# Optimization experiments

Hardware: AMD Instinct MI355X
Metric: run time of the kernel (lower is better)

The kernel has to match this reference:

```python
import jax, jax.numpy as jnp
import numpy as np


def gcn(adj_bin, x, W, b):
    # torch_geometric GCNConv with add_self_loops=True, no edge_weight (binary adj)
    N = adj_bin.shape[-1]
    A = adj_bin + jnp.eye(N, dtype=adj_bin.dtype)
    d = A.sum(-1)
    dis = jnp.where(d > 0, jax.lax.rsqrt(jnp.maximum(d, 1e-12)), 0.0)
    norm = dis[..., :, None] * A * dis[..., None, :]
    return jnp.einsum('bij,bjh->bih', norm, x @ W) + b


def normalize_batch_adj(adj):
    # CoarsenBlock.normalize_batch_adj on weighted dense adjacency
    N = adj.shape[-1]
    A = adj + jnp.eye(N, dtype=adj.dtype)
    dis = jnp.clip(A.sum(-1), 1.0, None) ** -0.5
    newA = dis[..., :, None] * A * dis[..., None, :]
    return (adj.sum(-1) > 0).astype(adj.dtype)[..., None] * newA


def cut_and_mask(alpha, num_sent, k):
    # get_topk_range_for_sentences: walk alpha in descending order until k
    # indices that are sentence nodes (index < num_sent) have been seen.
    N = alpha.shape[0]
    order = jnp.argsort(-alpha)  # descending
    csum = jnp.cumsum((order < num_sent).astype(jnp.int32))
    pos = jnp.argmax(csum >= k)  # first position where k sentences seen
    cut = alpha[order[pos]]
    sorted_mask = (jnp.arange(N) <= pos).astype(alpha.dtype)
    index_mask = jnp.zeros_like(alpha).at[order].set(sorted_mask)
    return cut, index_mask


def setup_inputs() -> dict:
    key = jax.random.key(0)
    ks = jax.random.split(key, 8)
    B, N, F, H = 16, 1024, 768, 128
    x = jax.random.normal(ks[0], (B, N, F), jnp.float32)
    w = jax.random.uniform(ks[1], (B, N, N), jnp.float32)
    m = jax.random.uniform(ks[2], (B, N, N)) < 0.03  # ~30 avg degree
    adj = jnp.where(m, w, 0.0)
    num_sentences = jax.random.randint(ks[3], (B,), 4, N + 1).astype(jnp.int32)
    W1 = jax.random.normal(ks[4], (F, H), jnp.float32) / np.float32(np.sqrt(F))
    b1 = jnp.zeros((H,), jnp.float32)
    Watt = jax.random.normal(ks[5], (H, 1), jnp.float32) / np.float32(np.sqrt(H))
    batt = jnp.zeros((1,), jnp.float32)
    W2 = jax.random.normal(ks[6], (H, F), jnp.float32) / np.float32(np.sqrt(H))
    b2 = jnp.zeros((F,), jnp.float32)
    return dict(x=x, adj=adj, num_sentences=num_sentences, W1=W1, b1=b1,
                Watt=Watt, batt=batt, W2=W2, b2=b2, num_output_sentences=3)


def reference(x, adj, num_sentences, W1, b1, Watt, batt, W2, b2, num_output_sentences):
    adj_bin = (adj > 0).astype(x.dtype)
    # embed_block1 + relu
    x1 = jax.nn.relu(gcn(adj_bin, x, W1, b1))  # [B,N,H]
    # attention: sigmoid(gcn_att(x1)^2)
    alpha = jax.nn.sigmoid(gcn(adj_bin, x1, Watt, batt) ** 2)[..., 0]  # [B,N]
    norm_adj = normalize_batch_adj(adj)  # [B,N,N]
    cut, index_mask = jax.vmap(cut_and_mask, in_axes=(0, 0, None))(
        alpha, num_sentences, num_output_sentences)
    cut_alpha = jax.nn.relu(alpha + 1e-7 - cut[:, None])  # [B,N]
    S = norm_adj * cut_alpha[:, None, :]
    # F.normalize(S, p=1, dim=-1)
    S = S / jnp.clip(jnp.abs(S).sum(-1, keepdims=True), 1e-12, None)
    # coarsening matmuls
    coarse_x = jnp.einsum('bij,bif->bjf', S, x1)        # S^T x1
    StA = jnp.einsum('bji,bjk->bik', S, adj)            # S^T A
    coarse_adj = jnp.einsum('bik,bkl->bil', StA, S)     # S^T A S
    coarse_adj = jnp.floor(coarse_adj * 1e4) / 1e4      # floor quantization, 4 digits
    # embed_block2 + tanh on the coarse graph (binary coarse adjacency)
    coarse_bin = (coarse_adj != 0).astype(x.dtype)
    x2 = jnp.tanh(gcn(coarse_bin, coarse_x, W2, b2))    # [B,N,F]
    xs0 = coarse_x.mean(-1)
    xs1 = x2.mean(-1)
    return (x2, coarse_x, coarse_adj, S, index_mask, xs0, xs1)
```

## Files before the change

### kernel.cpp

```cpp
#include <hip/hip_runtime.h>

#define B_ 16
#define N_ 1024
#define F_ 768
#define H_ 128

typedef float f32x4 __attribute__((ext_vector_type(4)));
typedef short s16x8 __attribute__((ext_vector_type(8)));
typedef unsigned short u16;
typedef u16 u16x8 __attribute__((ext_vector_type(8)));
typedef u16 u16x4 __attribute__((ext_vector_type(4)));
typedef unsigned long long u64;

__device__ __forceinline__ u16 f2b(float f) {
  unsigned u = __float_as_uint(f);
  unsigned r = (u + 0x7FFFu + ((u >> 16) & 1u)) >> 16;
  return (u16)r;
}
__device__ __forceinline__ float b2f(u16 u) {
  return __uint_as_float(((unsigned)u) << 16);
}

__device__ __forceinline__ void gload16(const u16* g, u16* l) {
  __builtin_amdgcn_global_load_lds(
      (const __attribute__((address_space(1))) unsigned int*)g,
      (__attribute__((address_space(3))) unsigned int*)l, 16, 0, 0);
}

__device__ __forceinline__ float ftanh(float z) {
  z = fminf(fmaxf(z, -10.0f), 10.0f);
  float e = __expf(2.0f * z);
  return (e - 1.0f) / (e + 1.0f);
}

__device__ __forceinline__ float blockReduceSum256(float v) {
  __shared__ float red[4];
  #pragma unroll
  for (int o = 32; o > 0; o >>= 1) v += __shfl_down(v, o, 64);
  if ((threadIdx.x & 63) == 0) red[threadIdx.x >> 6] = v;
  __syncthreads();
  float r = red[0] + red[1] + red[2] + red[3];
  __syncthreads();
  return r;
}

__global__ __launch_bounds__(256) void k_prep(
    const float* __restrict__ X, u16* __restrict__ Yh, u16* __restrict__ Ym,
    u16* __restrict__ Yl, long n4,
    const float* __restrict__ W1, u16* __restrict__ W1h,
    u16* __restrict__ W1m, u16* __restrict__ W1l,
    const float* __restrict__ adj, float* __restrict__ dis_bin,
    float* __restrict__ dr, float* __restrict__ dc, u64* __restrict__ bm,
    u16* __restrict__ adj_bf, int* __restrict__ rowcnt,
    float* __restrict__ xs0, float* __restrict__ xs1) {
  __shared__ float tile[32][33];
  int tid = threadIdx.x;
  if (blockIdx.x < 2048) {
    long i = (long)blockIdx.x * 256 + tid;
    long stride = 2048L * 256;
    for (; i < n4; i += stride) {
      f32x4 v = *(const f32x4*)(X + i * 4);
      u16x4 oh, om, ol;
      #pragma unroll
      for (int e = 0; e < 4; ++e) {
        float f = v[e];
        u16 h = f2b(f); float r1 = f - b2f(h);
        u16 m = f2b(r1); float r2 = r1 - b2f(m);
        u16 l = f2b(r2);
        oh[e] = h; om[e] = m; ol[e] = l;
      }
      *(u16x4*)(Yh + i * 4) = oh;
      *(u16x4*)(Ym + i * 4) = om;
      *(u16x4*)(Yl + i * 4) = ol;
    }
  } else if (blockIdx.x < 2144) {
    int bid = blockIdx.x - 2048;
    int bx = bid & 3, by = bid >> 2;
    int tx = tid & 31, ty = tid >> 5;
    int r0 = by * 32, c0 = bx * 32;
    #pragma unroll
    for (int i = 0; i < 4; ++i)
      tile[ty + i * 8][tx] = W1[(long)(r0 + ty + i * 8) * H_ + (c0 + tx)];
    __syncthreads();
    #pragma unroll
    for (int i = 0; i < 4; ++i) {
      float v = tile[tx][ty + i * 8];
      long o = (long)(c0 + ty + i * 8) * F_ + (r0 + tx);
      u16 h = f2b(v); float r1 = v - b2f(h);
      u16 m = f2b(r1); float r2 = r1 - b2f(m);
      u16 l = f2b(r2);
      W1h[o] = h; W1m[o] = m; W1l[o] = l;
    }
  } else {
    long row = blockIdx.x - 2144;
    const float* a = adj + row * N_;
    u16* ab = adj_bf + row * N_;
    float cnt = 0.f, sw = 0.f;
    #pragma unroll
    for (int it = 0; it < 4; ++it) {
      int j = tid + it * 256;
      float v = a[j];
      ab[j] = f2b(v);
      bool nz = (v != 0.0f);
      u64 ball = __ballot(nz);
      if ((tid & 63) == 0) bm[row * 16 + it * 4 + (tid >> 6)] = ball;
      if (nz) { cnt += 1.0f; sw += v; }
    }
    __shared__ float r1[4], r2[4];
    #pragma unroll
    for (int o = 32; o > 0; o >>= 1) { cnt += __shfl_down(cnt, o, 64); sw += __shfl_down(sw, o, 64); }
    if ((tid & 63) == 0) { r1[tid >> 6] = cnt; r2[tid >> 6] = sw; }
    __syncthreads();
    if (tid == 0) {
      float c = r1[0] + r1[1] + r1[2] + r1[3];
      float s = r2[0] + r2[1] + r2[2] + r2[3];
      dis_bin[row] = rsqrtf(c + 1.0f);
      float d = rsqrtf(s + 1.0f);
      dc[row] = d;
      dr[row] = (s > 0.0f) ? d : 0.0f;
      rowcnt[row] = 0;
      xs0[row] = 0.0f;
      xs1[row] = 0.0f;
    }
  }
}

template<int NPLANES, int MODE>
__global__ __launch_bounds__(256) void mgemmW(
    const u16* __restrict__ A0, const u16* __restrict__ A1, const u16* __restrict__ A2,
    const u16* __restrict__ B0, const u16* __restrict__ B1, const u16* __restrict__ B2,
    float* __restrict__ C, int N, int K, long sA, long sB, long sC,
    u16* __restrict__ Cbf, float* __restrict__ xsum) {
  int bz = blockIdx.z;
  int m0 = blockIdx.y * 128, n0 = blockIdx.x * 64;
  __shared__ __align__(16) u16 As[NPLANES][128 * 32];
  __shared__ __align__(16) u16 Bs[NPLANES][64 * 32];
  int tid = threadIdx.x;
  int lane = tid & 63, wave = tid >> 6;
  int wr = wave >> 1, wc = wave & 1;
  int kg = lane >> 4, r16 = lane & 15;
  const u16* Aps[3] = {A0, A1, A2};
  const u16* Bps[3] = {B0, B1, B2};
  const u16* ga[NPLANES];
  const u16* gb[NPLANES];
  #pragma unroll
  for (int p2 = 0; p2 < NPLANES; ++p2) {
    ga[p2] = Aps[p2] + (long)bz * sA + (long)(m0 + (tid >> 2)) * K + (tid & 3) * 8;
    gb[p2] = Bps[p2] + (long)bz * sB + (long)(n0 + (tid >> 2)) * K + (tid & 3) * 8;
  }
  f32x4 acc[4][2] = {};

  for (int k0 = 0; k0 < K; k0 += 32) {
    #pragma unroll
    for (int p2 = 0; p2 < NPLANES; ++p2) {
      gload16(ga[p2] + k0, &As[p2][tid * 8]);
      gload16(ga[p2] + (long)64 * K + k0, &As[p2][2048 + tid * 8]);
      gload16(gb[p2] + k0, &Bs[p2][tid * 8]);
    }
    __syncthreads();
    s16x8 af[NPLANES][4], bf[NPLANES][2];
    #pragma unroll
    for (int p2 = 0; p2 < NPLANES; ++p2) {
      #pragma unroll
      for (int m = 0; m < 4; ++m)
        af[p2][m] = *(const s16x8*)(&As[p2][(wr * 64 + m * 16 + r16) * 32 + kg * 8]);
      #pragma unroll
      for (int n = 0; n < 2; ++n)
        bf[p2][n] = *(const s16x8*)(&Bs[p2][(wc * 32 + n * 16 + r16) * 32 + kg * 8]);
    }
    #pragma unroll
    for (int m = 0; m < 4; ++m)
      #pragma unroll
      for (int n = 0; n < 2; ++n) {
        acc[m][n] = __builtin_amdgcn_mfma_f32_16x16x32_bf16(af[0][m], bf[0][n], acc[m][n], 0, 0, 0);
        if constexpr (NPLANES == 3) {
          acc[m][n] = __builtin_amdgcn_mfma_f32_16x16x32_bf16(af[0][m], bf[1][n], acc[m][n], 0, 0, 0);
          acc[m][n] = __builtin_amdgcn_mfma_f32_16x16x32_bf16(af[1][m], bf[0][n], acc[m][n], 0, 0, 0);
          acc[m][n] = __builtin_amdgcn_mfma_f32_16x16x32_bf16(af[1][m], bf[1][n], acc[m][n], 0, 0, 0);
          acc[m][n] = __builtin_amdgcn_mfma_f32_16x16x32_bf16(af[0][m], bf[2][n], acc[m][n], 0, 0, 0);
          acc[m][n] = __builtin_amdgcn_mfma_f32_16x16x32_bf16(af[2][m], bf[0][n], acc[m][n], 0, 0, 0);
        }
      }
    __syncthreads();
  }

  #pragma unroll
  for (int m = 0; m < 4; ++m)
    #pragma unroll
    for (int r = 0; r < 4; ++r) {
      int row = m0 + wr * 64 + m * 16 + kg * 4 + r;
      float part = 0.f;
      #pragma unroll
      for (int n = 0; n < 2; ++n) {
        int col = n0 + wc * 32 + n * 16 + r16;
        long cidx = (long)bz * sC + (long)row * N + col;
        float v = acc[m][n][r];
        C[cidx] = v;
        if constexpr (MODE == 1) { Cbf[cidx] = f2b(v); part += v; }
      }
      if constexpr (MODE == 1) {
        #pragma unroll
        for (int o2 = 1; o2 < 16; o2 <<= 1) part += __shfl_xor(part, o2, 64);
        if (r16 == 0) atomicAdd(&xsum[(long)bz * N_ + row], part * (1.0f / H_));
      }
    }
}

__global__ __launch_bounds__(256) void k_G5G6(
    const u16* __restrict__ St, const u16* __restrict__ x1T,
    float* __restrict__ out_cx, u16* __restrict__ cx_bf,
    float* __restrict__ xs0,
    const u16* __restrict__ adjBF, u16* __restrict__ M1t) {
  __shared__ __align__(16) u16 smem[128 * 64];
  const long NN = (long)N_ * N_;
  const long NH = (long)N_ * H_;
  int tid = threadIdx.x;
  int lane = tid & 63, wave = tid >> 6;
  int wr = wave >> 1, wc = wave & 1;
  int kg = lane >> 4, r16 = lane & 15;

  if ((int)blockIdx.x < 256) {
    int id = blockIdx.x;
    int bxg = id & 1, byg = (id >> 1) & 7, bz = id >> 4;
    int m0 = byg * 128, n0 = bxg * 64;
    u16* As = smem;
    u16* Bs = smem + 128 * 32;
    const u16* ga = St + (long)bz * NN + (long)(m0 + (tid >> 2)) * N_ + (tid & 3) * 8;
    const u16* gb = x1T + (long)bz * NH + (long)(n0 + (tid >> 2)) * N_ + (tid & 3) * 8;
    f32x4 acc[4][2] = {};
    for (int k0 = 0; k0 < N_; k0 += 32) {
      gload16(ga + k0, &As[tid * 8]);
      gload16(ga + (long)64 * N_ + k0, &As[2048 + tid * 8]);
      gload16(gb + k0, &Bs[tid * 8]);
      __syncthreads();
      s16x8 af[4], bf[2];
      #pragma unroll
      for (int m = 0; m < 4; ++m)
        af[m] = *(const s16x8*)(&As[(wr * 64 + m * 16 + r16) * 32 + kg * 8]);
      #pragma unroll
      for (int n = 0; n < 2; ++n)
        bf[n] = *(const s16x8*)(&Bs[(wc * 32 + n * 16 + r16) * 32 + kg * 8]);
      #pragma unroll
      for (int m = 0; m < 4; ++m)
        #pragma unroll
        for (int n = 0; n < 2; ++n)
          acc[m][n] = __builtin_amdgcn_mfma_f32_16x16x32_bf16(af[m], bf[n], acc[m][n], 0, 0, 0);
      __syncthreads();
    }
    #pragma unroll
    for (int m = 0; m < 4; ++m)
      #pragma unroll
      for (int r = 0; r < 4; ++r) {
        int row = m0 + wr * 64 + m * 16 + kg * 4 + r;
        float part = 0.f;
        #pragma unroll
        for (int n = 0; n < 2; ++n) {
          int col = n0 + wc * 32 + n * 16 + r16;
          long cidx = (long)bz * NH + (long)row * H_ + col;
          float v = acc[m][n][r];
          out_cx[cidx] = v;
          cx_bf[cidx] = f2b(v);
          part += v;
        }
        #pragma unroll
        for (int o2 = 1; o2 < 16; o2 <<= 1) part += __shfl_xor(part, o2, 64);
        if (r16 == 0) atomicAdd(&xs0[(long)bz * N_ + row], part * (1.0f / H_));
      }
  } else {
    int lin = (int)blockIdx.x - 256;
    int swz = (lin & 7) * 128 + (lin >> 3);
    int bx = swz & 7, by = (swz >> 3) & 7, bz = swz >> 6;
    int m0 = by * 128, n0 = bx * 128;
    u16* As = smem;
    u16* Bs = smem + 128 * 32;
    const u16* ga = St + (long)bz * NN + (long)(m0 + (tid >> 2)) * N_ + (tid & 3) * 8;
    const u16* gb = adjBF + (long)bz * NN + (long)(n0 + (tid >> 2)) * N_ + (tid & 3) * 8;
    f32x4 acc[4][4] = {};
    for (int k0 = 0; k0 < N_; k0 += 32) {
      gload16(ga + k0, &As[tid * 8]);
      gload16(ga + (long)64 * N_ + k0, &As[2048 + tid * 8]);
      gload16(gb + k0, &Bs[tid * 8]);
      gload16(gb + (long)64 * N_ + k0, &Bs[2048 + tid * 8]);
      __syncthreads();
      s16x8 af[4], bfr[4];
      #pragma unroll
      for (int m = 0; m < 4; ++m)
        af[m] = *(const s16x8*)(&As[(wr * 64 + m * 16 + r16) * 32 + kg * 8]);
      #pragma unroll
      for (int n = 0; n < 4; ++n)
        bfr[n] = *(const s16x8*)(&Bs[(wc * 64 + n * 16 + r16) * 32 + kg * 8]);
      #pragma unroll
      for (int m = 0; m < 4; ++m)
        #pragma unroll
        for (int n = 0; n < 4; ++n)
          acc[m][n] = __builtin_amdgcn_mfma_f32_16x16x32_bf16(af[m], bfr[n], acc[m][n], 0, 0, 0);
      __syncthreads();
    }
    #pragma unroll
    for (int m = 0; m < 4; ++m)
      #pragma unroll
      for (int r = 0; r < 4; ++r) {
        int row = m0 + wr * 64 + m * 16 + kg * 4 + r;
        #pragma unroll
        for (int n = 0; n < 4; ++n) {
          int col = n0 + wc * 64 + n * 16 + r16;
          M1t[(long)bz * NN + (long)row * N_ + col] = f2b(acc[m][n][r]);
        }
      }
  }
}

__global__ __launch_bounds__(256) void k_spmm_relu(
    const u64* __restrict__ bm, const float* __restrict__ P1,
    const float* __restrict__ dis_bin, const float* __restrict__ b1,
    const float* __restrict__ Watt, float* __restrict__ x1,
    float* __restrict__ t) {
  long row = blockIdx.x;
  int b = (int)(row >> 10), i = (int)(row & 1023);
  const float* Pb = P1 + (long)b * (long)N_ * H_;
  const float* db = dis_bin + (long)b * N_;
  __shared__ int idxs[N_];
  __shared__ int wtot[4];
  __shared__ float accs[H_];
  int tid = threadIdx.x;
  int wid = tid >> 6, lane = tid & 63;
  int base = tid * 4;
  u64 word = bm[row * 16 + (tid >> 4)];
  int sh = base & 63;
  int f0 = (int)((word >> sh) & 1), f1 = (int)((word >> (sh + 1)) & 1);
  int f2 = (int)((word >> (sh + 2)) & 1), f3 = (int)((word >> (sh + 3)) & 1);
  int c0 = f0 + f1 + f2 + f3;
  int inc = c0;
  #pragma unroll
  for (int o = 1; o < 64; o <<= 1) {
    int v = __shfl_up(inc, o, 64);
    if (lane >= o) inc += v;
  }
  if (lane == 63) wtot[wid] = inc;
  __syncthreads();
  int wbase = 0;
  #pragma unroll
  for (int w = 0; w < 4; ++w) wbase += (w < wid) ? wtot[w] : 0;
  int pos = wbase + inc - c0;
  int n = wtot[0] + wtot[1] + wtot[2] + wtot[3];
  if (f0) idxs[pos++] = base;
  if (f1) idxs[pos++] = base + 1;
  if (f2) idxs[pos++] = base + 2;
  if (f3) idxs[pos++] = base + 3;
  __syncthreads();
  int c = tid & 127, team = tid >> 7;
  float acc = 0.f;
  for (int u = team; u < n; u += 2) {
    int j = idxs[u];
    acc += db[j] * Pb[(long)j * H_ + c];
  }
  if (team == 1) accs[c] = acc;
  __syncthreads();
  float v = 0.f;
  if (team == 0) {
    float di = db[i];
    float tot = acc + accs[c] + di * Pb[(long)i * H_ + c];
    v = fmaxf(di * tot + b1[c], 0.0f);
    x1[row * H_ + c] = v;
  }
  __syncthreads();
  float prod = (team == 0) ? v * Watt[c] : 0.f;
  float s = blockReduceSum256(prod);
  if (tid == 0) t[row] = s;
}

__global__ __launch_bounds__(256) void k_alpha(
    const u64* __restrict__ bm, const float* __restrict__ dis_bin,
    const float* __restrict__ t, const float* __restrict__ batt,
    float* __restrict__ alpha) {
  long row = blockIdx.x;
  int b = (int)(row >> 10), i = (int)(row & 1023);
  const float* db = dis_bin + (long)b * N_;
  const float* tb = t + (long)b * N_;
  int tid = threadIdx.x;
  float s = 0.f;
  #pragma unroll
  for (int it = 0; it < 4; ++it) {
    int j = tid + it * 256;
    u64 word = bm[row * 16 + (j >> 6)];
    if ((word >> (j & 63)) & 1) s += db[j] * tb[j];
  }
  s = blockReduceSum256(s);
  if (tid == 0) {
    float di = db[i];
    float pre = di * (s + di * tb[i]) + batt[0];
    float z = pre * pre;
    alpha[row] = 1.0f / (1.0f + expf(-z));
  }
}

__global__ __launch_bounds__(1024) void k_cutmask2(
    const float* __restrict__ alpha, const int* __restrict__ num_sent,
    const int* __restrict__ nout, float* __restrict__ index_mask,
    float* __restrict__ ca) {
  int b = blockIdx.x, tid = threadIdx.x;
  __shared__ u64 keys[N_];
  __shared__ u64 red[N_];
  int ns = num_sent[b];
  float av = alpha[(long)b * N_ + tid];
  unsigned bits = __float_as_uint(av);
  u64 keyFull = ((u64)bits << 32) | (u64)(0xFFFFFFFFu - (unsigned)tid);
  keys[tid] = (tid < ns) ? keyFull : 0ULL;
  __syncthreads();
  int k = nout[0];
  u64 cutkey = 0;
  for (int r = 0; r < k; ++r) {
    red[tid] = keys[tid];
    __syncthreads();
    for (int off = 512; off > 0; off >>= 1) {
      if (tid < off) { u64 o = red[tid + off]; if (o > red[tid]) red[tid] = o; }
      __syncthreads();
    }
    u64 mx = red[0];
    __syncthreads();
    if (r == k - 1) cutkey = mx;
    else if (keys[tid] == mx) keys[tid] = 0ULL;
    __syncthreads();
  }
  float cutalpha = __uint_as_float((unsigned)(cutkey >> 32));
  index_mask[(long)b * N_ + tid] = (keyFull >= cutkey) ? 1.0f : 0.0f;
  ca[(long)b * N_ + tid] = fmaxf(av + 1e-7f - cutalpha, 0.0f);
}

__global__ __launch_bounds__(256) void k_build_S(
    const u16* __restrict__ abf, const float* __restrict__ dr,
    const float* __restrict__ dc, const float* __restrict__ ca,
    float* __restrict__ S) {
  long row = blockIdx.x;
  int b = (int)(row >> 10), i = (int)(row & 1023);
  const u16* a = abf + row * N_;
  const float* dcb = dc + (long)b * N_;
  const float* cab = ca + (long)b * N_;
  float dri = dr[row];
  int tid = threadIdx.x;
  u16x4 av4 = *(const u16x4*)(a + tid * 4);
  f32x4 dc4 = *(const f32x4*)(dcb + tid * 4);
  f32x4 ca4 = *(const f32x4*)(cab + tid * 4);
  float ls = 0.f;
  f32x4 pv;
  #pragma unroll
  for (int e = 0; e < 4; ++e) {
    int j = tid * 4 + e;
    float avv = b2f(av4[e]) + ((j == i) ? 1.0f : 0.0f);
    float v = dri * avv * dc4[e] * ca4[e];
    pv[e] = v;
    ls += v;
  }
  float sum = blockReduceSum256(ls);
  float denom = fmaxf(sum, 1e-12f);
  f32x4 out;
  #pragma unroll
  for (int e = 0; e < 4; ++e) out[e] = pv[e] / denom;
  *(f32x4*)(&S[row * N_ + tid * 4]) = out;
}

__device__ __forceinline__ void convT_body(
    const float* __restrict__ Xb, u16* __restrict__ Yb, int R, int C,
    int r0, int c0, float tile[32][33]) {
  int tx = threadIdx.x & 31, ty = threadIdx.x >> 5;
  #pragma unroll
  for (int i = 0; i < 4; ++i)
    tile[ty + i * 8][tx] = Xb[(long)(r0 + ty + i * 8) * C + (c0 + tx)];
  __syncthreads();
  #pragma unroll
  for (int i = 0; i < 4; ++i)
    Yb[(long)(c0 + ty + i * 8) * R + (r0 + tx)] = f2b(tile[tx][ty + i * 8]);
}

__global__ __launch_bounds__(256) void k_convTall(
    const float* __restrict__ S, u16* __restrict__ St,
    const float* __restrict__ x1, u16* __restrict__ x1T,
    const float* __restrict__ W2, u16* __restrict__ W2T) {
  __shared__ float tile[32][33];
  long NN = (long)N_ * N_;
  long NH = (long)N_ * H_;
  int id = blockIdx.x;
  if (id < 16384) {
    int bx = id & 31, by = (id >> 5) & 31, bz = id >> 10;
    convT_body(S + (long)bz * NN, St + (long)bz * NN, N_, N_, by * 32, bx * 32, tile);
  } else if (id < 18432) {
    int id2 = id - 16384;
    int bx = id2 & 3, by = (id2 >> 2) & 31, bz = id2 >> 7;
    convT_body(x1 + (long)bz * NH, x1T + (long)bz * NH, N_, H_, by * 32, bx * 32, tile);
  } else {
    int id3 = id - 18432;
    int bx = id3 % 24, by = id3 / 24;
    convT_body(W2, W2T, H_, F_, by * 32, bx * 32, tile);
  }
}

template<int MODE>
__global__ __launch_bounds__(256) void mgemm(
    const u16* __restrict__ A, const u16* __restrict__ Bt, void* __restrict__ Cv,
    int M, int N, int K, long sA, long sB, long sC, long ldb,
    const int* __restrict__ cnt, const float* __restrict__ bias,
    int* __restrict__ rowcnt, u16* __restrict__ cbin,
    float* __restrict__ xsum) {
  int gx = gridDim.x, gy = gridDim.y;
  int lin = (blockIdx.z * gy + blockIdx.y) * gx + blockIdx.x;
  int total = gx * gy * gridDim.z;
  int chunk = total >> 3;
  int swz = (lin & 7) * chunk + (lin >> 3);
  int bx = swz % gx; int t2 = swz / gx; int by = t2 % gy; int bz = t2 / gy;

  int m0 = by * 128, n0 = bx * 128;
  const u16* Ab = A + (long)bz * sA + (long)m0 * K;
  const u16* Bb = Bt + (long)bz * sB + (long)n0 * ldb;
  __shared__ __align__(16) u16 As[128 * 32];
  __shared__ __align__(16) u16 Bs[128 * 32];
  int tid = threadIdx.x;
  int lane = tid & 63, wave = tid >> 6;
  int wr = wave >> 1, wc = wave & 1;
  int kg = lane >> 4, r16 = lane & 15;
  const u16* ga = Ab + (long)(tid >> 2) * K + (tid & 3) * 8;
  const u16* gb = Bb + (long)(tid >> 2) * ldb + (tid & 3) * 8;
  f32x4 acc[4][4] = {};

  for (int k0 = 0; k0 < K; k0 += 32) {
    gload16(ga + k0, &As[tid * 8]);
    gload16(ga + (long)64 * K + k0, &As[2048 + tid * 8]);
    gload16(gb + k0, &Bs[tid * 8]);
    gload16(gb + (long)64 * ldb + k0, &Bs[2048 + tid * 8]);
    __syncthreads();
    s16x8 af[4], bfr[4];
    #pragma unroll
    for (int m = 0; m < 4; ++m)
      af[m] = *(const s16x8*)(&As[(wr * 64 + m * 16 + r16) * 32 + kg * 8]);
    #pragma unroll
    for (int n = 0; n < 4; ++n)
      bfr[n] = *(const s16x8*)(&Bs[(wc * 64 + n * 16 + r16) * 32 + kg * 8]);
    #pragma unroll
    for (int m = 0; m < 4; ++m)
      #pragma unroll
      for (int n = 0; n < 4; ++n)
        acc[m][n] = __builtin_amdgcn_mfma_f32_16x16x32_bf16(af[m], bfr[n], acc[m][n], 0, 0, 0);
    __syncthreads();
  }

  if constexpr (MODE == 2) {
    int* cntl = (int*)As;
    if (tid < 128) cntl[tid] = 0;
    __syncthreads();
    #pragma unroll
    for (int m = 0; m < 4; ++m) {
      #pragma unroll
      for (int r = 0; r < 4; ++r) {
        int lrow = wr * 64 + m * 16 + kg * 4 + r;
        int row = m0 + lrow;
        int nz = 0;
        #pragma unroll
        for (int n = 0; n < 4; ++n) {
          int col = n0 + wc * 64 + n * 16 + r16;
          float q = floorf(acc[m][n][r] * 10000.0f) / 10000.0f;
          long cidx = (long)bz * sC + (long)row * N + col;
          ((float*)Cv)[cidx] = q;
          bool qnz = (q != 0.0f);
          u16 bv;
          if (row == col) bv = qnz ? (u16)0x4000 : (u16)0x3F80;
          else            bv = qnz ? (u16)0x3F80 : (u16)0;
          cbin[cidx] = bv;
          nz += qnz ? 1 : 0;
        }
        atomicAdd(&cntl[lrow], nz);
      }
    }
    __syncthreads();
    if (tid < 128) atomicAdd(&rowcnt[(long)bz * N_ + m0 + tid], cntl[tid]);
    return;
  }

  #pragma unroll
  for (int m = 0; m < 4; ++m) {
    #pragma unroll
    for (int r = 0; r < 4; ++r) {
      int row = m0 + wr * 64 + m * 16 + kg * 4 + r;
      float sc = 0.f;
      if constexpr (MODE == 3)
        sc = rsqrtf(1.0f + (float)cnt[(long)bz * N_ + row]);
      float part = 0.f;
      #pragma unroll
      for (int n = 0; n < 4; ++n) {
        int col = n0 + wc * 64 + n * 16 + r16;
        float v = acc[m][n][r];
        long cidx = (long)bz * sC + (long)row * N + col;
        if constexpr (MODE == 3) {
          float th = ftanh(sc * v + bias[col]);
          ((float*)Cv)[cidx] = th;
          part += th;
        } else if constexpr (MODE == 5) {
          float scc = rsqrtf(1.0f + (float)cnt[col]);
          ((u16*)Cv)[cidx] = f2b(scc * v);
        } else {
          ((float*)Cv)[cidx] = v;
        }
      }
      if constexpr (MODE == 3) {
        #pragma unroll
        for (int o2 = 1; o2 < 16; o2 <<= 1) part += __shfl_xor(part, o2, 64);
        if (r16 == 0) atomicAdd(&xsum[(long)bz * N_ + row], part * (1.0f / F_));
      }
    }
  }
}

extern "C" void kernel_launch(void* const* d_in, const int* in_sizes, int n_in,
                              void* d_out, int out_size, void* d_ws, size_t ws_size,
                              hipStream_t stream) {
  const float* x     = (const float*)d_in[0];
  const float* adj   = (const float*)d_in[1];
  const int*   nsent = (const int*)d_in[2];
  const float* W1    = (const float*)d_in[3];
  const float* b1    = (const float*)d_in[4];
  const float* Watt  = (const float*)d_in[5];
  const float* batt  = (const float*)d_in[6];
  const float* W2    = (const float*)d_in[7];
  const float* b2    = (const float*)d_in[8];
  const int*   nout  = (const int*)d_in[9];

  const long NN = (long)N_ * N_;
  const long NH = (long)N_ * H_;
  const long NF = (long)N_ * F_;
  const int BN = B_ * N_;

  float* out_x2   = (float*)d_out;
  float* out_cx   = out_x2 + (long)B_ * NF;
  float* out_cadj = out_cx + (long)B_ * NH;
  float* out_S    = out_cadj + (long)B_ * NN;
  float* out_im   = out_S + (long)B_ * NN;
  float* out_xs0  = out_im + BN;
  float* out_xs1  = out_xs0 + BN;

  char* wsb = (char*)d_ws;
  float* P1      = (float*)wsb;
  float* x1      = P1 + (long)B_ * NH;
  float* t       = x1 + (long)B_ * NH;
  float* alpha   = t + BN;
  float* dis_bin = alpha + BN;
  float* dr      = dis_bin + BN;
  float* dc      = dr + BN;
  float* ca      = dc + BN;
  int*   rowcnt  = (int*)(ca + BN);
  u64*   bm      = (u64*)(rowcnt + BN);
  char*  p       = (char*)(bm + (long)BN * 16);
  p = (char*)(((size_t)p + 255) & ~(size_t)255);
  u16* W1h   = (u16*)p;  p += (long)H_ * F_ * 2;
  u16* W1m   = (u16*)p;  p += (long)H_ * F_ * 2;
  u16* W1l   = (u16*)p;  p += (long)H_ * F_ * 2;
  u16* W2T   = (u16*)p;  p += (long)H_ * F_ * 2;
  u16* PT    = (u16*)p;  p += (long)B_ * NH * 2;
  u16* St    = (u16*)p;  p += (long)B_ * NN * 2;
  u16* wsB   = (u16*)p;  p += (long)B_ * NN * 2;
  u16* xl3   = (u16*)p;
  u16* xh    = St;
  u16* xm    = wsB;
  u16* xl    = xl3;
  u16* cx_bf = (u16*)P1;
  u16* x1T   = PT;
  u16* adjBF = (u16*)out_cadj;
  u16* cbin  = wsB;
  u16* P2T   = St;
  u16* M1t   = (u16*)out_x2;

  k_prep<<<dim3(2144 + BN), dim3(256), 0, stream>>>(
      x, xh, xm, xl, (long)B_ * NF / 4, W1, W1h, W1m, W1l,
      adj, dis_bin, dr, dc, bm, adjBF, rowcnt, out_xs0, out_xs1);

  mgemmW<3, 0><<<dim3(H_ / 64, BN / 128, 1), dim3(256), 0, stream>>>(
      xh, xm, xl, W1h, W1m, W1l, P1, H_, F_, 0, 0, 0, nullptr, nullptr);

  k_spmm_relu<<<dim3(BN), dim3(256), 0, stream>>>(bm, P1, dis_bin, b1, Watt, x1, t);

  k_alpha<<<dim3(BN), dim3(256), 0, stream>>>(bm, dis_bin, t, batt, alpha);
  k_cutmask2<<<dim3(B_), dim3(1024), 0, stream>>>(alpha, nsent, nout, out_im, ca);
  k_build_S<<<dim3(BN), dim3(256), 0, stream>>>(adjBF, dr, dc, ca, out_S);

  k_convTall<<<dim3(16384 + 2048 + 96), dim3(256), 0, stream>>>(
      out_S, St, x1, x1T, W2, W2T);

  k_G5G6<<<dim3(256 + 1024), dim3(256), 0, stream>>>(
      St, x1T, out_cx, cx_bf, out_xs0, adjBF, M1t);

  mgemm<2><<<dim3(N_ / 128, N_ / 128, B_), dim3(256), 0, stream>>>(
      St, M1t, out_cadj, N_, N_, N_, NN, NN, NN, N_, nullptr, nullptr, rowcnt,
      cbin, nullptr);

  mgemm<5><<<dim3(BN / 128, F_ / 128, 1), dim3(256), 0, stream>>>(
      W2T, cx_bf, P2T, F_, BN, H_, 0, 0, 0, H_, rowcnt, nullptr, nullptr,
      nullptr, nullptr);

  mgemm<3><<<dim3(F_ / 128, N_ / 128, B_), dim3(256), 0, stream>>>(
      cbin, P2T, out_x2, N_, F_, N_, NN, N_, NF, (long)BN, rowcnt, b2,
      nullptr, nullptr, out_xs1);
}
```

Baseline: 391.4 us.

## Fuse fp32-to-bf16x3 split of x into the first GEMM's A-tile load

Removes the separate pass in the prep kernel that split x into three bf16 planes in global memory, and instead loads fp32 x tiles directly in the first GEMM and splits them into hi/mid/lo planes in shared memory. This avoids writing and rereading three bf16 copies of the large feature matrix. In exchange, the A tile now goes through synchronous register loads and per-element conversion inside the K loop, and each x tile is read once per column block. The A tile uses a padded row pitch in LDS.

```diff
diff --git a/kernel.cpp b/kernel.cpp
--- a/kernel.cpp
+++ b/kernel.cpp
@@ -45,8 +45,6 @@
 }
 
 __global__ __launch_bounds__(256) void k_prep(
-    const float* __restrict__ X, u16* __restrict__ Yh, u16* __restrict__ Ym,
-    u16* __restrict__ Yl, long n4,
     const float* __restrict__ W1, u16* __restrict__ W1h,
     u16* __restrict__ W1m, u16* __restrict__ W1l,
     const float* __restrict__ adj, float* __restrict__ dis_bin,
@@ -55,26 +53,8 @@
     float* __restrict__ xs0, float* __restrict__ xs1) {
   __shared__ float tile[32][33];
   int tid = threadIdx.x;
-  if (blockIdx.x < 2048) {
-    long i = (long)blockIdx.x * 256 + tid;
-    long stride = 2048L * 256;
-    for (; i < n4; i += stride) {
-      f32x4 v = *(const f32x4*)(X + i * 4);
-      u16x4 oh, om, ol;
-      #pragma unroll
-      for (int e = 0; e < 4; ++e) {
-        float f = v[e];
-        u16 h = f2b(f); float r1 = f - b2f(h);
-        u16 m = f2b(r1); float r2 = r1 - b2f(m);
-        u16 l = f2b(r2);
-        oh[e] = h; om[e] = m; ol[e] = l;
-      }
-      *(u16x4*)(Yh + i * 4) = oh;
-      *(u16x4*)(Ym + i * 4) = om;
-      *(u16x4*)(Yl + i * 4) = ol;
-    }
-  } else if (blockIdx.x < 2144) {
-    int bid = blockIdx.x - 2048;
+  if (blockIdx.x < 96) {
+    int bid = blockIdx.x;
     int bx = bid & 3, by = bid >> 2;
     int tx = tid & 31, ty = tid >> 5;
     int r0 = by * 32, c0 = bx * 32;
@@ -92,7 +72,7 @@
       W1h[o] = h; W1m[o] = m; W1l[o] = l;
     }
   } else {
-    long row = blockIdx.x - 2144;
+    long row = blockIdx.x - 96;
     const float* a = adj + row * N_;
     u16* ab = adj_bf + row * N_;
     float cnt = 0.f, sw = 0.f;
@@ -125,45 +105,53 @@
   }
 }
 
-template<int NPLANES, int MODE>
-__global__ __launch_bounds__(256) void mgemmW(
-    const u16* __restrict__ A0, const u16* __restrict__ A1, const u16* __restrict__ A2,
-    const u16* __restrict__ B0, const u16* __restrict__ B1, const u16* __restrict__ B2,
-    float* __restrict__ C, int N, int K, long sA, long sB, long sC,
-    u16* __restrict__ Cbf, float* __restrict__ xsum) {
-  int bz = blockIdx.z;
+__global__ __launch_bounds__(256) void mgemmG1(
+    const float* __restrict__ X,
+    const u16* __restrict__ B0, const u16* __restrict__ B1,
+    const u16* __restrict__ B2, float* __restrict__ C) {
   int m0 = blockIdx.y * 128, n0 = blockIdx.x * 64;
-  __shared__ __align__(16) u16 As[NPLANES][128 * 32];
-  __shared__ __align__(16) u16 Bs[NPLANES][64 * 32];
+  __shared__ __align__(16) u16 As[3][128 * 40];
+  __shared__ __align__(16) u16 Bs[3][64 * 32];
   int tid = threadIdx.x;
   int lane = tid & 63, wave = tid >> 6;
   int wr = wave >> 1, wc = wave & 1;
   int kg = lane >> 4, r16 = lane & 15;
-  const u16* Aps[3] = {A0, A1, A2};
-  const u16* Bps[3] = {B0, B1, B2};
-  const u16* ga[NPLANES];
-  const u16* gb[NPLANES];
-  #pragma unroll
-  for (int p2 = 0; p2 < NPLANES; ++p2) {
-    ga[p2] = Aps[p2] + (long)bz * sA + (long)(m0 + (tid >> 2)) * K + (tid & 3) * 8;
-    gb[p2] = Bps[p2] + (long)bz * sB + (long)(n0 + (tid >> 2)) * K + (tid & 3) * 8;
-  }
+  int arow = tid >> 1, ahalf = (tid & 1) * 16;
+  const float* gx = X + (long)(m0 + arow) * F_ + ahalf;
+  const u16* gb[3] = {
+      B0 + (long)(n0 + (tid >> 2)) * F_ + (tid & 3) * 8,
+      B1 + (long)(n0 + (tid >> 2)) * F_ + (tid & 3) * 8,
+      B2 + (long)(n0 + (tid >> 2)) * F_ + (tid & 3) * 8};
   f32x4 acc[4][2] = {};
 
-  for (int k0 = 0; k0 < K; k0 += 32) {
-    #pragma unroll
-    for (int p2 = 0; p2 < NPLANES; ++p2) {
-      gload16(ga[p2] + k0, &As[p2][tid * 8]);
-      gload16(ga[p2] + (long)64 * K + k0, &As[p2][2048 + tid * 8]);
+  for (int k0 = 0; k0 < F_; k0 += 32) {
+    #pragma unroll
+    for (int p2 = 0; p2 < 3; ++p2)
       gload16(gb[p2] + k0, &Bs[p2][tid * 8]);
-    }
-    __syncthreads();
-    s16x8 af[NPLANES][4], bf[NPLANES][2];
-    #pragma unroll
-    for (int p2 = 0; p2 < NPLANES; ++p2) {
+    #pragma unroll
+    for (int q = 0; q < 4; ++q) {
+      f32x4 v = *(const f32x4*)(gx + k0 + q * 4);
+      u16x4 oh, om, ol;
+      #pragma unroll
+      for (int e = 0; e < 4; ++e) {
+        float f = v[e];
+        u16 h = f2b(f); float rr1 = f - b2f(h);
+        u16 m = f2b(rr1); float rr2 = rr1 - b2f(m);
+        u16 l = f2b(rr2);
+        oh[e] = h; om[e] = m; ol[e] = l;
+      }
+      int off = arow * 40 + ahalf + q * 4;
+      *(u16x4*)(&As[0][off]) = oh;
+      *(u16x4*)(&As[1][off]) = om;
+      *(u16x4*)(&As[2][off]) = ol;
+    }
+    __syncthreads();
+    s16x8 af[3][4], bf[3][2];
+    #pragma unroll
+    for (int p2 = 0; p2 < 3; ++p2) {
       #pragma unroll
       for (int m = 0; m < 4; ++m)
-        af[p2][m] = *(const s16x8*)(&As[p2][(wr * 64 + m * 16 + r16) * 32 + kg * 8]);
+        af[p2][m] = *(const s16x8*)(&As[p2][(wr * 64 + m * 16 + r16) * 40 + kg * 8]);
       #pragma unroll
       for (int n = 0; n < 2; ++n)
         bf[p2][n] = *(const s16x8*)(&Bs[p2][(wc * 32 + n * 16 + r16) * 32 + kg * 8]);
@@ -173,13 +161,11 @@
       #pragma unroll
       for (int n = 0; n < 2; ++n) {
         acc[m][n] = __builtin_amdgcn_mfma_f32_16x16x32_bf16(af[0][m], bf[0][n], acc[m][n], 0, 0, 0);
-        if constexpr (NPLANES == 3) {
-          acc[m][n] = __builtin_amdgcn_mfma_f32_16x16x32_bf16(af[0][m], bf[1][n], acc[m][n], 0, 0, 0);
-          acc[m][n] = __builtin_amdgcn_mfma_f32_16x16x32_bf16(af[1][m], bf[0][n], acc[m][n], 0, 0, 0);
-          acc[m][n] = __builtin_amdgcn_mfma_f32_16x16x32_bf16(af[1][m], bf[1][n], acc[m][n], 0, 0, 0);
-          acc[m][n] = __builtin_amdgcn_mfma_f32_16x16x32_bf16(af[0][m], bf[2][n], acc[m][n], 0, 0, 0);
-          acc[m][n] = __builtin_amdgcn_mfma_f32_16x16x32_bf16(af[2][m], bf[0][n], acc[m][n], 0, 0, 0);
-        }
+        acc[m][n] = __builtin_amdgcn_mfma_f32_16x16x32_bf16(af[0][m], bf[1][n], acc[m][n], 0, 0, 0);
+        acc[m][n] = __builtin_amdgcn_mfma_f32_16x16x32_bf16(af[1][m], bf[0][n], acc[m][n], 0, 0, 0);
+        acc[m][n] = __builtin_amdgcn_mfma_f32_16x16x32_bf16(af[1][m], bf[1][n], acc[m][n], 0, 0, 0);
+        acc[m][n] = __builtin_amdgcn_mfma_f32_16x16x32_bf16(af[0][m], bf[2][n], acc[m][n], 0, 0, 0);
+        acc[m][n] = __builtin_amdgcn_mfma_f32_16x16x32_bf16(af[2][m], bf[0][n], acc[m][n], 0, 0, 0);
       }
     __syncthreads();
   }
@@ -189,19 +175,10 @@
     #pragma unroll
     for (int r = 0; r < 4; ++r) {
       int row = m0 + wr * 64 + m * 16 + kg * 4 + r;
-      float part = 0.f;
       #pragma unroll
       for (int n = 0; n < 2; ++n) {
         int col = n0 + wc * 32 + n * 16 + r16;
-        long cidx = (long)bz * sC + (long)row * N + col;
-        float v = acc[m][n][r];
-        C[cidx] = v;
-        if constexpr (MODE == 1) { Cbf[cidx] = f2b(v); part += v; }
-      }
-      if constexpr (MODE == 1) {
-        #pragma unroll
-        for (int o2 = 1; o2 < 16; o2 <<= 1) part += __shfl_xor(part, o2, 64);
-        if (r16 == 0) atomicAdd(&xsum[(long)bz * N_ + row], part * (1.0f / H_));
+        C[(long)row * H_ + col] = acc[m][n][r];
       }
     }
 }
@@ -655,10 +632,6 @@
   u16* PT    = (u16*)p;  p += (long)B_ * NH * 2;
   u16* St    = (u16*)p;  p += (long)B_ * NN * 2;
   u16* wsB   = (u16*)p;  p += (long)B_ * NN * 2;
-  u16* xl3   = (u16*)p;
-  u16* xh    = St;
-  u16* xm    = wsB;
-  u16* xl    = xl3;
   u16* cx_bf = (u16*)P1;
   u16* x1T   = PT;
   u16* adjBF = (u16*)out_cadj;
@@ -666,12 +639,12 @@
   u16* P2T   = St;
   u16* M1t   = (u16*)out_x2;
 
-  k_prep<<<dim3(2144 + BN), dim3(256), 0, stream>>>(
-      x, xh, xm, xl, (long)B_ * NF / 4, W1, W1h, W1m, W1l,
+  k_prep<<<dim3(96 + BN), dim3(256), 0, stream>>>(
+      W1, W1h, W1m, W1l,
       adj, dis_bin, dr, dc, bm, adjBF, rowcnt, out_xs0, out_xs1);
 
-  mgemmW<3, 0><<<dim3(H_ / 64, BN / 128, 1), dim3(256), 0, stream>>>(
-      xh, xm, xl, W1h, W1m, W1l, P1, H_, F_, 0, 0, 0, nullptr, nullptr);
+  mgemmG1<<<dim3(H_ / 64, BN / 128, 1), dim3(256), 0, stream>>>(
+      x, W1h, W1m, W1l, P1);
 
   k_spmm_relu<<<dim3(BN), dim3(256), 0, stream>>>(bm, P1, dis_bin, b1, Watt, x1, t);
 
```

Result: no change. 383.9 us (-1.9%).
